# Optimization experiments

Hardware: AMD Instinct MI355X
Metric: run time of the kernel (lower is better)

The kernel has to match this reference:

```python
import jax, jax.numpy as jnp
import numpy as np

EMBED = 100
BATCH = 4096
NUM_NEG = 256
U, P, W, RP, B, C = 30000, 50000, 100000, 50000, 5000, 1000


def _tab(k, v, e=EMBED):
    r = 0.5 / e
    w = jax.random.uniform(k, (v + 1, e), minval=-r, maxval=r, dtype=jnp.float32)
    return w.at[-1].set(0.0)  # padding row is zeros, as in torch code


def setup_inputs() -> dict:
    key = jax.random.key(0)
    ks = jax.random.split(key, 10)
    inp = {
        'user_emb': _tab(ks[0], U),
        'product_emb': _tab(ks[1], P),
        'word_emb': _tab(ks[2], W),
        'brand_emb': _tab(ks[3], B),
        'category_emb': _tab(ks[4], C),
        'rproduct_emb': _tab(ks[5], RP),
        'rel_vecs': jax.random.uniform(ks[6], (8, EMBED), minval=-0.5 / EMBED, maxval=0.5 / EMBED, dtype=jnp.float32),
        'purchase_bias': jnp.zeros((P + 1,), jnp.float32),
        'mentions_bias': jnp.zeros((W + 1,), jnp.float32),
        'describe_bias': jnp.zeros((W + 1,), jnp.float32),
        'produced_bias': jnp.zeros((B + 1,), jnp.float32),
        'belongs_bias': jnp.zeros((C + 1,), jnp.float32),
        'also_bought_bias': jnp.zeros((RP + 1,), jnp.float32),
        'also_viewed_bias': jnp.zeros((RP + 1,), jnp.float32),
        'together_bias': jnp.zeros((RP + 1,), jnp.float32),
    }
    # batch_idxs columns: (u, p, w, b, c, rp1, rp2, rp3), each in its own vocab range
    col_max = [U, P, W, B, C, RP, RP, RP]
    cols = [jax.random.randint(jax.random.fold_in(ks[7], i), (BATCH,), 0, m) for i, m in enumerate(col_max)]
    inp['batch_idxs'] = jnp.stack(cols, axis=1)
    # deterministic stand-in for torch.multinomial negative sampling, one row per relation
    neg_max = [P, W, W, B, C, RP, RP, RP]
    negs = [jax.random.randint(jax.random.fold_in(ks[8], i), (NUM_NEG,), 0, m) for i, m in enumerate(neg_max)]
    inp['neg_idxs'] = jnp.stack(negs, axis=0)
    return inp


def _neg_loss(head_tab, tail_tab, rvec, bias_tab, h, t, n):
    hv = head_tab[h]                      # [B,E] gather
    ex = hv + rvec                        # [B,E]
    tv = tail_tab[t]                      # [B,E]
    bias = bias_tab[t]                    # [B]
    pos = jnp.sum(ex * tv, axis=-1) + bias  # bmm([B,1,E],[B,E,1]) == rowwise dot
    nv = tail_tab[n]                      # [N,E]
    neg = jnp.einsum('be,ne->bn', ex, nv) + bias[:, None]  # [B,N]
    pos_loss = -jax.nn.log_sigmoid(pos)   # == -log(sigmoid(pos)), stable
    neg_loss = -jax.nn.log_sigmoid(-neg).sum(axis=1)
    return (pos_loss + neg_loss).mean()


def reference(batch_idxs, neg_idxs, user_emb, product_emb, word_emb, brand_emb,
              category_emb, rproduct_emb, rel_vecs, purchase_bias, mentions_bias,
              describe_bias, produced_bias, belongs_bias, also_bought_bias,
              also_viewed_bias, together_bias):
    # (head_tab, tail_tab, bias_tab, head_col, tail_col) per relation, in original order
    rels = [
        (user_emb, product_emb, purchase_bias, 0, 1),
        (user_emb, word_emb, mentions_bias, 0, 2),
        (product_emb, word_emb, describe_bias, 1, 2),
        (product_emb, brand_emb, produced_bias, 1, 3),
        (product_emb, category_emb, belongs_bias, 1, 4),
        (product_emb, rproduct_emb, also_bought_bias, 1, 5),
        (product_emb, rproduct_emb, also_viewed_bias, 1, 6),
        (product_emb, rproduct_emb, together_bias, 1, 7),
    ]
    loss = jnp.float32(0.0)
    for r, (ht, tt, bt, hc, tc) in enumerate(rels):
        loss = loss + _neg_loss(ht, tt, rel_vecs[r], bt,
                                batch_idxs[:, hc], batch_idxs[:, tc], neg_idxs[r])
    return loss
```

## Files before the change

kernel.cpp:

```cpp
#include <hip/hip_runtime.h>


#define EMBED   100
#define BATCH   4096
#define NUM_NEG 256
#define BM      128
#define BN      128
#define PITCH   128

typedef __attribute__((ext_vector_type(8))) short s8;
typedef __attribute__((ext_vector_type(4))) short s4;
typedef __attribute__((ext_vector_type(4))) float f4;

struct RelP {
    const float* head;
    const float* tail;
    const float* bias;
    int hc, tc;
};

struct Params {
    RelP rel[8];
    const float* rel_vecs;
    const int*   batch_idxs;
    const int*   neg_idxs;
    float*       out;
};

__device__ __forceinline__ float softplus_f(float x) {
    float e = __expf(-fabsf(x));
    return fmaxf(x, 0.0f) + __logf(1.0f + e);
}

__device__ __forceinline__ unsigned short bf16_rne(float f) {
    unsigned u = __float_as_uint(f);
    u += 0x7FFFu + ((u >> 16) & 1u);
    return (unsigned short)(u >> 16);
}

__launch_bounds__(256, 2)
__global__ void ke_kernel(Params p) {
    const int bid = blockIdx.x;
    const int r   = bid & 7;
    const int rb  = (bid >> 3) & 31;
    const int nb  = bid >> 8;
    const int tid = threadIdx.x;

    __shared__ __align__(16) short As[BM * PITCH];
    __shared__ __align__(16) short Bs[BN * PITCH];

    const RelP rp = p.rel[r];

    {
        const bool isA = tid < BM;
        const float* src;
        unsigned short extra;
        if (isA) {
            const int grow = rb * BM + tid;
            const int h  = p.batch_idxs[grow * 8 + rp.hc];
            const int ti = p.batch_idxs[grow * 8 + rp.tc];
            src   = rp.head + (size_t)h * EMBED;
            extra = bf16_rne(rp.bias[ti]);
        } else {
            const int n = p.neg_idxs[r * NUM_NEG + nb * BN + (tid - BM)];
            src   = rp.tail + (size_t)n * EMBED;
            extra = 0x3F80;
        }
        short* dst = isA ? (As + tid * PITCH) : (Bs + (tid - BM) * PITCH);
        const float4* s4p = (const float4*)src;
        const float4* rv4 = (const float4*)(p.rel_vecs + r * EMBED);

#pragma unroll
        for (int j = 0; j < 12; ++j) {
            float4 f0 = s4p[2 * j];
            float4 f1 = s4p[2 * j + 1];
            if (isA) {
                const float4 a = rv4[2 * j];
                const float4 b = rv4[2 * j + 1];
                f0.x += a.x; f0.y += a.y; f0.z += a.z; f0.w += a.w;
                f1.x += b.x; f1.y += b.y; f1.z += b.z; f1.w += b.w;
            }
            s8 v = { (short)bf16_rne(f0.x), (short)bf16_rne(f0.y),
                     (short)bf16_rne(f0.z), (short)bf16_rne(f0.w),
                     (short)bf16_rne(f1.x), (short)bf16_rne(f1.y),
                     (short)bf16_rne(f1.z), (short)bf16_rne(f1.w) };
            *(s8*)(dst + 8 * j) = v;
        }
        {
            float4 f = s4p[24];
            if (isA) {
                const float4 a = rv4[24];
                f.x += a.x; f.y += a.y; f.z += a.z; f.w += a.w;
            }
            s4 v = { (short)bf16_rne(f.x), (short)bf16_rne(f.y),
                     (short)bf16_rne(f.z), (short)bf16_rne(f.w) };
            *(s4*)(dst + 96) = v;
        }
        {
            s4 v = { (short)extra, 0, 0, 0 };
            *(s4*)(dst + 100) = v;
            s4 z = { 0, 0, 0, 0 };
#pragma unroll
            for (int j = 0; j < 6; ++j)
                *(s4*)(dst + 104 + 4 * j) = z;
        }
    }
    __syncthreads();

    const int wave = tid >> 6;
    const int lane = tid & 63;
    const int li   = lane & 15;
    const int q    = lane >> 4;
    const int wm   = wave >> 1;
    const int wn   = wave & 1;

    f4 acc[4][4];
#pragma unroll
    for (int i = 0; i < 4; ++i)
#pragma unroll
        for (int j = 0; j < 4; ++j)
            acc[i][j] = (f4){0.f, 0.f, 0.f, 0.f};

    const short* Abase = As + (wm * 64 + li) * PITCH + q * 8;
    const short* Bbase = Bs + (wn * 64 + li) * PITCH + q * 8;

#pragma unroll
    for (int s = 0; s < 4; ++s) {
        const s8 a0 = *(const s8*)(Abase +  0 * PITCH + s * 32);
        const s8 a1 = *(const s8*)(Abase + 16 * PITCH + s * 32);
        const s8 a2 = *(const s8*)(Abase + 32 * PITCH + s * 32);
        const s8 a3 = *(const s8*)(Abase + 48 * PITCH + s * 32);
        const s8 b0 = *(const s8*)(Bbase +  0 * PITCH + s * 32);
        const s8 b1 = *(const s8*)(Bbase + 16 * PITCH + s * 32);
        const s8 b2 = *(const s8*)(Bbase + 32 * PITCH + s * 32);
        const s8 b3 = *(const s8*)(Bbase + 48 * PITCH + s * 32);
        acc[0][0] = __builtin_amdgcn_mfma_f32_16x16x32_bf16(a0, b0, acc[0][0], 0, 0, 0);
        acc[0][1] = __builtin_amdgcn_mfma_f32_16x16x32_bf16(a0, b1, acc[0][1], 0, 0, 0);
        acc[0][2] = __builtin_amdgcn_mfma_f32_16x16x32_bf16(a0, b2, acc[0][2], 0, 0, 0);
        acc[0][3] = __builtin_amdgcn_mfma_f32_16x16x32_bf16(a0, b3, acc[0][3], 0, 0, 0);
        acc[1][0] = __builtin_amdgcn_mfma_f32_16x16x32_bf16(a1, b0, acc[1][0], 0, 0, 0);
        acc[1][1] = __builtin_amdgcn_mfma_f32_16x16x32_bf16(a1, b1, acc[1][1], 0, 0, 0);
        acc[1][2] = __builtin_amdgcn_mfma_f32_16x16x32_bf16(a1, b2, acc[1][2], 0, 0, 0);
        acc[1][3] = __builtin_amdgcn_mfma_f32_16x16x32_bf16(a1, b3, acc[1][3], 0, 0, 0);
        acc[2][0] = __builtin_amdgcn_mfma_f32_16x16x32_bf16(a2, b0, acc[2][0], 0, 0, 0);
        acc[2][1] = __builtin_amdgcn_mfma_f32_16x16x32_bf16(a2, b1, acc[2][1], 0, 0, 0);
        acc[2][2] = __builtin_amdgcn_mfma_f32_16x16x32_bf16(a2, b2, acc[2][2], 0, 0, 0);
        acc[2][3] = __builtin_amdgcn_mfma_f32_16x16x32_bf16(a2, b3, acc[2][3], 0, 0, 0);
        acc[3][0] = __builtin_amdgcn_mfma_f32_16x16x32_bf16(a3, b0, acc[3][0], 0, 0, 0);
        acc[3][1] = __builtin_amdgcn_mfma_f32_16x16x32_bf16(a3, b1, acc[3][1], 0, 0, 0);
        acc[3][2] = __builtin_amdgcn_mfma_f32_16x16x32_bf16(a3, b2, acc[3][2], 0, 0, 0);
        acc[3][3] = __builtin_amdgcn_mfma_f32_16x16x32_bf16(a3, b3, acc[3][3], 0, 0, 0);
    }

    float local = 0.0f;
#pragma unroll
    for (int i = 0; i < 4; ++i)
#pragma unroll
        for (int j = 0; j < 4; ++j) {
            local += softplus_f(acc[i][j].x);
            local += softplus_f(acc[i][j].y);
            local += softplus_f(acc[i][j].z);
            local += softplus_f(acc[i][j].w);
        }

    if (nb == 0 && tid < BM) {
        const int row = rb * BM + tid;
        const int h = p.batch_idxs[row * 8 + rp.hc];
        const int t = p.batch_idxs[row * 8 + rp.tc];
        const float4* __restrict__ hv  = (const float4*)(rp.head + (size_t)h * EMBED);
        const float4* __restrict__ rv4 = (const float4*)(p.rel_vecs + r * EMBED);
        const float4* __restrict__ tv  = (const float4*)(rp.tail + (size_t)t * EMBED);
        float d0 = 0.f, d1 = 0.f, d2 = 0.f, d3 = 0.f;
#pragma unroll
        for (int j = 0; j < EMBED / 4; ++j) {
            const float4 a = hv[j];
            const float4 b = rv4[j];
            const float4 v = tv[j];
            d0 = fmaf(a.x + b.x, v.x, d0);
            d1 = fmaf(a.y + b.y, v.y, d1);
            d2 = fmaf(a.z + b.z, v.z, d2);
            d3 = fmaf(a.w + b.w, v.w, d3);
        }
        const float pos = ((d0 + d1) + (d2 + d3)) + rp.bias[t];
        local += softplus_f(-pos);
    }

#pragma unroll
    for (int off = 32; off > 0; off >>= 1)
        local += __shfl_down(local, off, 64);

    __syncthreads();
    float* wsum = (float*)As;
    if (lane == 0) wsum[wave] = local;
    __syncthreads();
    if (tid == 0) {
        const float s = (wsum[0] + wsum[1]) + (wsum[2] + wsum[3]);
        atomicAdd(p.out, s * (1.0f / BATCH));
    }
}

extern "C" void kernel_launch(void* const* d_in, const int* in_sizes, int n_in,
                              void* d_out, int out_size, void* d_ws, size_t ws_size,
                              hipStream_t stream) {
    const float* user  = (const float*)d_in[0];
    const float* prod  = (const float*)d_in[1];
    const float* word  = (const float*)d_in[2];
    const float* brand = (const float*)d_in[3];
    const float* cat   = (const float*)d_in[4];
    const float* rprod = (const float*)d_in[5];

    Params p;
    p.rel_vecs   = (const float*)d_in[6];
    p.batch_idxs = (const int*)d_in[15];
    p.neg_idxs   = (const int*)d_in[16];
    p.out        = (float*)d_out;

    p.rel[0] = {user, prod,  (const float*)d_in[7],  0, 1};
    p.rel[1] = {user, word,  (const float*)d_in[8],  0, 2};
    p.rel[2] = {prod, word,  (const float*)d_in[9],  1, 2};
    p.rel[3] = {prod, brand, (const float*)d_in[10], 1, 3};
    p.rel[4] = {prod, cat,   (const float*)d_in[11], 1, 4};
    p.rel[5] = {prod, rprod, (const float*)d_in[12], 1, 5};
    p.rel[6] = {prod, rprod, (const float*)d_in[13], 1, 6};
    p.rel[7] = {prod, rprod, (const float*)d_in[14], 1, 7};

    hipMemsetAsync(d_out, 0, sizeof(float), stream);
    ke_kernel<<<512, 256, 0, stream>>>(p);
}
```

Measured before the change: 155.2 us.

## Halve A tile to 64 rows, double grid, reuse staged head rows for positive score

Reduces the batch tile from 128 to 64 rows, doubling the grid to 1024 blocks and raising the occupancy hint to 3 blocks per SIMD. The last wave, now idle during staging, prefetches the positive tail index and bias and later computes the positive dot from the bf16 head+relation rows already in shared memory instead of re-gathering from global memory. This cuts redundant global gathers and spreads work across more CUs, at the cost of re-gathering B rows twice as often and computing the positive score in bf16 instead of fp32.

```diff
diff --git a/kernel.cpp b/kernel.cpp
--- a/kernel.cpp
+++ b/kernel.cpp
@@ -4,7 +4,7 @@
 #define EMBED   100
 #define BATCH   4096
 #define NUM_NEG 256
-#define BM      128
+#define BM      64
 #define BN      128
 #define PITCH   128
 
@@ -38,12 +38,16 @@
     return (unsigned short)(u >> 16);
 }
 
-__launch_bounds__(256, 2)
+__device__ __forceinline__ float bf16_to_f(short s) {
+    return __uint_as_float(((unsigned)(unsigned short)s) << 16);
+}
+
+__launch_bounds__(256, 3)
 __global__ void ke_kernel(Params p) {
     const int bid = blockIdx.x;
     const int r   = bid & 7;
-    const int rb  = (bid >> 3) & 31;
-    const int nb  = bid >> 8;
+    const int rb  = (bid >> 3) & 63;
+    const int nb  = bid >> 9;
     const int tid = threadIdx.x;
 
     __shared__ __align__(16) short As[BM * PITCH];
@@ -51,22 +55,24 @@
 
     const RelP rp = p.rel[r];
 
-    {
+    if (tid < 192) {
         const bool isA = tid < BM;
         const float* src;
         unsigned short extra;
+        short* dst;
         if (isA) {
             const int grow = rb * BM + tid;
             const int h  = p.batch_idxs[grow * 8 + rp.hc];
             const int ti = p.batch_idxs[grow * 8 + rp.tc];
             src   = rp.head + (size_t)h * EMBED;
             extra = bf16_rne(rp.bias[ti]);
+            dst   = As + tid * PITCH;
         } else {
             const int n = p.neg_idxs[r * NUM_NEG + nb * BN + (tid - BM)];
             src   = rp.tail + (size_t)n * EMBED;
             extra = 0x3F80;
-        }
-        short* dst = isA ? (As + tid * PITCH) : (Bs + (tid - BM) * PITCH);
+            dst   = Bs + (tid - BM) * PITCH;
+        }
         const float4* s4p = (const float4*)src;
         const float4* rv4 = (const float4*)(p.rel_vecs + r * EMBED);
 
@@ -105,31 +111,41 @@
                 *(s4*)(dst + 104 + 4 * j) = z;
         }
     }
+
+    const bool doPos = (nb == 0) && (tid >= 192);
+    const int  prow  = rb * BM + (tid - 192);
+    int   pt   = 0;
+    const float* ptail = rp.tail;
+    float pbias = 0.0f;
+    if (doPos) {
+        pt    = p.batch_idxs[prow * 8 + rp.tc];
+        ptail = rp.tail + (size_t)pt * EMBED;
+        pbias = rp.bias[pt];
+    }
+
     __syncthreads();
 
     const int wave = tid >> 6;
     const int lane = tid & 63;
     const int li   = lane & 15;
     const int q    = lane >> 4;
-    const int wm   = wave >> 1;
-    const int wn   = wave & 1;
-
-    f4 acc[4][4];
-#pragma unroll
-    for (int i = 0; i < 4; ++i)
+    const int wm   = wave & 1;
+    const int wn   = wave >> 1;
+
+    f4 acc[2][4];
+#pragma unroll
+    for (int i = 0; i < 2; ++i)
 #pragma unroll
         for (int j = 0; j < 4; ++j)
             acc[i][j] = (f4){0.f, 0.f, 0.f, 0.f};
 
-    const short* Abase = As + (wm * 64 + li) * PITCH + q * 8;
+    const short* Abase = As + (wm * 32 + li) * PITCH + q * 8;
     const short* Bbase = Bs + (wn * 64 + li) * PITCH + q * 8;
 
 #pragma unroll
     for (int s = 0; s < 4; ++s) {
         const s8 a0 = *(const s8*)(Abase +  0 * PITCH + s * 32);
         const s8 a1 = *(const s8*)(Abase + 16 * PITCH + s * 32);
-        const s8 a2 = *(const s8*)(Abase + 32 * PITCH + s * 32);
-        const s8 a3 = *(const s8*)(Abase + 48 * PITCH + s * 32);
         const s8 b0 = *(const s8*)(Bbase +  0 * PITCH + s * 32);
         const s8 b1 = *(const s8*)(Bbase + 16 * PITCH + s * 32);
         const s8 b2 = *(const s8*)(Bbase + 32 * PITCH + s * 32);
@@ -142,19 +158,11 @@
         acc[1][1] = __builtin_amdgcn_mfma_f32_16x16x32_bf16(a1, b1, acc[1][1], 0, 0, 0);
         acc[1][2] = __builtin_amdgcn_mfma_f32_16x16x32_bf16(a1, b2, acc[1][2], 0, 0, 0);
         acc[1][3] = __builtin_amdgcn_mfma_f32_16x16x32_bf16(a1, b3, acc[1][3], 0, 0, 0);
-        acc[2][0] = __builtin_amdgcn_mfma_f32_16x16x32_bf16(a2, b0, acc[2][0], 0, 0, 0);
-        acc[2][1] = __builtin_amdgcn_mfma_f32_16x16x32_bf16(a2, b1, acc[2][1], 0, 0, 0);
-        acc[2][2] = __builtin_amdgcn_mfma_f32_16x16x32_bf16(a2, b2, acc[2][2], 0, 0, 0);
-        acc[2][3] = __builtin_amdgcn_mfma_f32_16x16x32_bf16(a2, b3, acc[2][3], 0, 0, 0);
-        acc[3][0] = __builtin_amdgcn_mfma_f32_16x16x32_bf16(a3, b0, acc[3][0], 0, 0, 0);
-        acc[3][1] = __builtin_amdgcn_mfma_f32_16x16x32_bf16(a3, b1, acc[3][1], 0, 0, 0);
-        acc[3][2] = __builtin_amdgcn_mfma_f32_16x16x32_bf16(a3, b2, acc[3][2], 0, 0, 0);
-        acc[3][3] = __builtin_amdgcn_mfma_f32_16x16x32_bf16(a3, b3, acc[3][3], 0, 0, 0);
     }
 
     float local = 0.0f;
 #pragma unroll
-    for (int i = 0; i < 4; ++i)
+    for (int i = 0; i < 2; ++i)
 #pragma unroll
         for (int j = 0; j < 4; ++j) {
             local += softplus_f(acc[i][j].x);
@@ -163,25 +171,20 @@
             local += softplus_f(acc[i][j].w);
         }
 
-    if (nb == 0 && tid < BM) {
-        const int row = rb * BM + tid;
-        const int h = p.batch_idxs[row * 8 + rp.hc];
-        const int t = p.batch_idxs[row * 8 + rp.tc];
-        const float4* __restrict__ hv  = (const float4*)(rp.head + (size_t)h * EMBED);
-        const float4* __restrict__ rv4 = (const float4*)(p.rel_vecs + r * EMBED);
-        const float4* __restrict__ tv  = (const float4*)(rp.tail + (size_t)t * EMBED);
+    if (doPos) {
+        const short* exr = As + (tid - 192) * PITCH;
+        const float4* tv = (const float4*)ptail;
         float d0 = 0.f, d1 = 0.f, d2 = 0.f, d3 = 0.f;
 #pragma unroll
-        for (int j = 0; j < EMBED / 4; ++j) {
-            const float4 a = hv[j];
-            const float4 b = rv4[j];
+        for (int j = 0; j < 25; ++j) {
+            const s4 e = *(const s4*)(exr + 4 * j);
             const float4 v = tv[j];
-            d0 = fmaf(a.x + b.x, v.x, d0);
-            d1 = fmaf(a.y + b.y, v.y, d1);
-            d2 = fmaf(a.z + b.z, v.z, d2);
-            d3 = fmaf(a.w + b.w, v.w, d3);
-        }
-        const float pos = ((d0 + d1) + (d2 + d3)) + rp.bias[t];
+            d0 = fmaf(bf16_to_f(e.x), v.x, d0);
+            d1 = fmaf(bf16_to_f(e.y), v.y, d1);
+            d2 = fmaf(bf16_to_f(e.z), v.z, d2);
+            d3 = fmaf(bf16_to_f(e.w), v.w, d3);
+        }
+        const float pos = ((d0 + d1) + (d2 + d3)) + pbias;
         local += softplus_f(-pos);
     }
 
@@ -190,7 +193,7 @@
         local += __shfl_down(local, off, 64);
 
     __syncthreads();
-    float* wsum = (float*)As;
+    float* wsum = (float*)Bs;
     if (lane == 0) wsum[wave] = local;
     __syncthreads();
     if (tid == 0) {
@@ -225,5 +228,5 @@
     p.rel[7] = {prod, rprod, (const float*)d_in[14], 1, 7};
 
     hipMemsetAsync(d_out, 0, sizeof(float), stream);
-    ke_kernel<<<512, 256, 0, stream>>>(p);
-}
+    ke_kernel<<<1024, 256, 0, stream>>>(p);
+}
```

Measured after the change: 164.8 us. +6.1%, slower.
